# Kernel tuning notes

Hardware: AMD Instinct MI355X
Metric: run time of the kernel (lower is better)

Reference implementation:

```python
import jax, jax.numpy as jnp
import numpy as np

L, N, D_IN = 4, 2048, 1024
H, DH = 8, 64
INNER = H * DH          # 512
D_OUT = D_IN            # out_dim defaults to input_dim
SCALE = DH ** -0.5


def setup_inputs() -> dict:
    key = jax.random.key(0)
    ks = jax.random.split(key, 7)
    x = jax.random.normal(ks[0], (L, N, D_IN), jnp.float32)
    # torch Linear weights are [out_features, in_features]; xavier-ish scale
    Wq = jax.random.normal(ks[1], (INNER, D_IN), jnp.float32) * 0.03
    Wk = jax.random.normal(ks[2], (INNER, D_IN), jnp.float32) * 0.03
    Wv = jax.random.normal(ks[3], (INNER, D_IN), jnp.float32) * 0.03
    Wo = jax.random.normal(ks[4], (D_OUT, INNER), jnp.float32) * 0.03
    bo = jnp.zeros((D_OUT,), jnp.float32)
    # boolean key-padding mask [L, n]; ensure at least one valid key per row
    mask = jax.random.uniform(ks[5], (L, N)) < 0.9
    mask = mask.at[:, 0].set(True)
    return {"x": x, "Wq": Wq, "Wk": Wk, "Wv": Wv, "Wo": Wo, "bo": bo, "mask": mask}


def reference(x, Wq, Wk, Wv, Wo, bo, mask):
    # projections (Linear: y = x @ W^T), split heads: L n (h d) -> l h n d
    def split_heads(t):
        return t.reshape(L, N, H, DH).transpose(0, 2, 1, 3)

    q = split_heads(jnp.einsum('lnd,ed->lne', x, Wq))
    k = split_heads(jnp.einsum('lnd,ed->lne', x, Wk))  # context defaults to x
    v = split_heads(jnp.einsum('lnd,ed->lne', x, Wv))

    sim = jnp.einsum('lhnd,lhmd->lhnm', q, k) * SCALE   # [L,H,N,N]
    neg = -jnp.finfo(sim.dtype).max
    sim = jnp.where(mask[:, None, None, :], sim, neg)   # mask over key dim
    attn = jax.nn.softmax(sim, axis=-1)

    out = jnp.einsum('lhnm,lhmd->lhnd', attn, v)        # [L,H,N,DH]
    out = out.transpose(0, 2, 1, 3).reshape(L, N, INNER)
    return out @ Wo.T + bo                               # [L,N,D_OUT]
```

## Files before the change

### kernel.cpp

```cpp
#include <hip/hip_runtime.h>
#include <hip/hip_bf16.h>

#define L_DIM 4
#define N_DIM 2048
#define DIN   1024
#define H_DIM 8
#define DH    64
#define INNER 512

typedef __attribute__((ext_vector_type(8))) short short8;
typedef __attribute__((ext_vector_type(4))) float f32x4;

__device__ __forceinline__ unsigned short f2bf(float f) {
  unsigned u = __builtin_bit_cast(unsigned, f);
  u += 0x7fffu + ((u >> 16) & 1u);
  return (unsigned short)(u >> 16);
}

__device__ __forceinline__ unsigned pack2(float a, float b) {
  unsigned ua = __builtin_bit_cast(unsigned, a) + 0x8000u;
  unsigned ub = __builtin_bit_cast(unsigned, b) + 0x8000u;
  return (ua >> 16) | (ub & 0xffff0000u);
}

typedef __attribute__((address_space(3))) unsigned int lds_uint;
typedef const __attribute__((address_space(1))) unsigned int glob_uint;
__device__ __forceinline__ void gl_lds16(const unsigned short* g,
                                         unsigned short* l) {
  __builtin_amdgcn_global_load_lds((glob_uint*)g, (lds_uint*)l, 16, 0, 0);
}

__global__ void cast_all(const float* __restrict__ x,
                         const float* __restrict__ wq,
                         const float* __restrict__ wk,
                         const float* __restrict__ wv,
                         const float* __restrict__ wo,
                         unsigned short* __restrict__ xb,
                         unsigned short* __restrict__ w3,
                         unsigned short* __restrict__ wob,
                         const unsigned char* __restrict__ mraw,
                         float* __restrict__ bias) {
  __shared__ int votes[2];
  int bid = blockIdx.x, t = threadIdx.x;
  if (bid == 10240) {
    if (t < 2) votes[t] = 0;
    __syncthreads();
    const unsigned int* m32 = (const unsigned int*)mraw;
    int anyf = 0, any8 = 0;
    for (int i = t; i < 2048; i += 256) {
      unsigned w = m32[i];
      if (w == 0x3f800000u) anyf = 1;
      if (w & 0xffffff00u) any8 = 1;
    }
    if (anyf) atomicOr(&votes[0], 1);
    if (any8) atomicOr(&votes[1], 1);
    __syncthreads();
    int fmt = votes[0] ? 2 : (votes[1] ? 1 : 0);
    for (int i = t; i < L_DIM * N_DIM; i += 256) {
      int mv;
      if (fmt == 2)      mv = ((const float*)mraw)[i] != 0.0f;
      else if (fmt == 1) mv = mraw[i] != 0;
      else               mv = ((const int*)mraw)[i] != 0;
      bias[i] = mv ? 0.0f : -1e30f;
    }
    return;
  }
  int i = (bid * 256 + t) * 4;
  const float* src; unsigned short* dst; int off;
  if (i < 8388608)      { src = x;  dst = xb;           off = i; }
  else if (i < 8912896) { src = wq; dst = w3;           off = i - 8388608; }
  else if (i < 9437184) { src = wk; dst = w3 + 524288;  off = i - 8912896; }
  else if (i < 9961472) { src = wv; dst = w3 + 1048576; off = i - 9437184; }
  else                  { src = wo; dst = wob;          off = i - 9961472; }
  float4 f = *(const float4*)(src + off);
  ushort4 o4;
  o4.x = f2bf(f.x); o4.y = f2bf(f.y); o4.z = f2bf(f.z); o4.w = f2bf(f.w);
  *(ushort4*)(dst + off) = o4;
}

__launch_bounds__(256, 3)
__global__ void gemm_qkv(const unsigned short* __restrict__ xb,
                         const unsigned short* __restrict__ w3,
                         unsigned short* __restrict__ qp,
                         unsigned short* __restrict__ kp,
                         unsigned short* __restrict__ vtp) {
  __shared__ __align__(16) unsigned short Sh[8704];
  unsigned short* As = Sh;
  unsigned short* Bs = Sh + 4096;
  const int tid = threadIdx.x, lane = tid & 63, wid = tid >> 6;
  const int l16 = lane & 15, quad = lane >> 4;
  const int wm = wid >> 1, wn = wid & 1;
  const int m0 = blockIdx.x * 128, n0 = blockIdx.y * 128;

  f32x4 acc[4][4] = {};
  for (int kt = 0; kt < DIN; kt += 32) {
    __syncthreads();
#pragma unroll
    for (int it = 0; it < 2; ++it) {
      int c = it * 256 + wid * 64 + lane;
      int row = c >> 2, kseg = c & 3;
      unsigned short* lbase = &As[(it * 256 + wid * 64) * 8];
      gl_lds16(&xb[(m0 + row) * DIN + kt + kseg * 8], lbase);
      unsigned short* lbase2 = &Bs[(it * 256 + wid * 64) * 8];
      gl_lds16(&w3[(n0 + row) * DIN + kt + kseg * 8], lbase2);
    }
    __syncthreads();
    short8 af[4], bf[4];
#pragma unroll
    for (int mt = 0; mt < 4; ++mt)
      af[mt] = *(const short8*)&As[(wm * 64 + mt * 16 + l16) * 32 + quad * 8];
#pragma unroll
    for (int nt = 0; nt < 4; ++nt)
      bf[nt] = *(const short8*)&Bs[(wn * 64 + nt * 16 + l16) * 32 + quad * 8];
#pragma unroll
    for (int mt = 0; mt < 4; ++mt)
#pragma unroll
      for (int nt = 0; nt < 4; ++nt)
        acc[mt][nt] = __builtin_amdgcn_mfma_f32_16x16x32_bf16(
            af[mt], bf[nt], acc[mt][nt], 0, 0, 0);
  }
  if (blockIdx.y >= 8) {
    const int l = m0 >> 11, mloc = m0 & 2047;
#pragma unroll
    for (int chunk = 0; chunk < 2; ++chunk) {
      __syncthreads();
      if (wn == chunk) {
#pragma unroll
        for (int mt = 0; mt < 4; ++mt)
#pragma unroll
          for (int nt = 0; nt < 4; ++nt) {
            int col = nt * 16 + l16;
            int rowb = wm * 64 + mt * 16 + quad * 4;
            ushort4 pv;
            pv.x = f2bf(acc[mt][nt][0]);
            pv.y = f2bf(acc[mt][nt][1]);
            pv.z = f2bf(acc[mt][nt][2]);
            pv.w = f2bf(acc[mt][nt][3]);
            *(ushort4*)&Sh[col * 136 + rowb] = pv;
          }
      }
      __syncthreads();
      int hh = ((n0 + chunk * 64) & 511) >> 6;
#pragma unroll
      for (int it = 0; it < 4; ++it) {
        int c = it * 256 + tid;
        int cl = c >> 4, seg = c & 15;
        short8 vv = *(const short8*)&Sh[cl * 136 + seg * 8];
        *(short8*)&vtp[((size_t)((l * H_DIM + hh) * DH + cl)) * N_DIM + mloc +
                       seg * 8] = vv;
      }
    }
  } else {
#pragma unroll
    for (int mt = 0; mt < 4; ++mt)
#pragma unroll
      for (int nt = 0; nt < 4; ++nt)
#pragma unroll
        for (int r = 0; r < 4; ++r) {
          int grow = m0 + wm * 64 + mt * 16 + quad * 4 + r;
          int gcol = n0 + wn * 64 + nt * 16 + l16;
          unsigned short bv = f2bf(acc[mt][nt][r]);
          int h = (gcol & 511) >> 6, d = gcol & 63;
          int l = grow >> 11, n = grow & 2047;
          unsigned short* dst = (gcol >> 9) ? kp : qp;
          dst[(((l * H_DIM + h) * N_DIM + n) * DH) + d] = bv;
        }
  }
}

#define PW_S 64
__launch_bounds__(256, 2)
__global__ void attn_kernel(const unsigned short* __restrict__ qg,
                            const unsigned short* __restrict__ kg,
                            const unsigned short* __restrict__ vtg,
                            const float* __restrict__ bias,
                            unsigned short* __restrict__ aout) {
  __shared__ __align__(16) unsigned short Ks[2][128 * 64];
  __shared__ __align__(16) unsigned short Vs[2][64 * 128];
  __shared__ __align__(16) unsigned short Pw[128 * PW_S];
  const int tid = threadIdx.x, lane = tid & 63, wid = tid >> 6;
  const int l16 = lane & 15, quad = lane >> 4;
  const int bid = blockIdx.x;
  const int xcd = bid & 7, j = bid >> 3;
  const int lh = xcd * 4 + (j >> 4);
  const int q0 = (j & 15) << 7;
  const int l = lh >> 3, h = lh & 7;
  const unsigned short* Qb = qg + (size_t)lh * N_DIM * DH;
  const unsigned short* Kb = kg + (size_t)lh * N_DIM * DH;
  const unsigned short* Vt = vtg + (size_t)lh * DH * N_DIM;
  const float* bl = bias + l * N_DIM;

  short8 qf[2][2];
#pragma unroll
  for (int mt = 0; mt < 2; ++mt)
#pragma unroll
    for (int ks = 0; ks < 2; ++ks)
      qf[mt][ks] = *(const short8*)&Qb[(q0 + wid * 32 + mt * 16 + l16) * DH +
                                       ks * 32 + quad * 8];

  f32x4 o[2][4] = {};
  float lsum[2] = {0.f, 0.f};

#pragma unroll
  for (int it = 0; it < 4; ++it) {
    int cb = it * 256 + wid * 64;
    int c = cb + lane;
    int key = c >> 3, sl = c & 7, gs = (sl + key) & 7;
    gl_lds16(&Kb[key * DH + gs * 8], &Ks[0][cb * 8]);
    int d = c >> 4, sv = c & 15, gv = (sv + d) & 15;
    gl_lds16(&Vt[(size_t)d * N_DIM + gv * 8], &Vs[0][cb * 8]);
  }

  for (int t = 0; t < 16; ++t) {
    const int kv = t << 7, buf = t & 1;
    __syncthreads();
    if (t < 15) {
      int kv2 = kv + 128, b2 = buf ^ 1;
#pragma unroll
      for (int it = 0; it < 4; ++it) {
        int cb = it * 256 + wid * 64;
        int c = cb + lane;
        int key = c >> 3, sl = c & 7, gs = (sl + key) & 7;
        gl_lds16(&Kb[(kv2 + key) * DH + gs * 8], &Ks[b2][cb * 8]);
        int d = c >> 4, sv = c & 15, gv = (sv + d) & 15;
        gl_lds16(&Vt[(size_t)d * N_DIM + kv2 + gv * 8], &Vs[b2][cb * 8]);
      }
    }
    const unsigned short* Kst = Ks[buf];
    const unsigned short* Vst = Vs[buf];

#pragma unroll
    for (int hf = 0; hf < 2; ++hf) {
      f32x4 sc[2][4] = {};
#pragma unroll
      for (int nt = 0; nt < 4; ++nt)
#pragma unroll
        for (int ks = 0; ks < 2; ++ks) {
          int s = (ks * 4 + quad - l16) & 7;
          short8 kf = *(const short8*)&Kst[(hf * 64 + nt * 16 + l16) * 64 +
                                           s * 8];
#pragma unroll
          for (int mt = 0; mt < 2; ++mt)
            sc[mt][nt] = __builtin_amdgcn_mfma_f32_16x16x32_bf16(
                kf, qf[mt][ks], sc[mt][nt], 0, 0, 0);
        }
#pragma unroll
      for (int mt = 0; mt < 2; ++mt) {
        unsigned short* pr = &Pw[(wid * 32 + mt * 16 + l16) * PW_S];
#pragma unroll
        for (int nt = 0; nt < 4; ++nt) {
          float4 b4 = *(const float4*)&bl[kv + hf * 64 + nt * 16 + quad * 4];
          float p0 = __expf(fmaf(sc[mt][nt][0], 0.125f, b4.x));
          float p1 = __expf(fmaf(sc[mt][nt][1], 0.125f, b4.y));
          float p2 = __expf(fmaf(sc[mt][nt][2], 0.125f, b4.z));
          float p3 = __expf(fmaf(sc[mt][nt][3], 0.125f, b4.w));
          lsum[mt] += (p0 + p1) + (p2 + p3);
          uint2 pk = make_uint2(pack2(p0, p1), pack2(p2, p3));
          int gk = nt * 2 + (quad >> 1);
          int s = (gk + l16) & 7;
          *(uint2*)&pr[s * 8 + (quad & 1) * 4] = pk;
        }
      }
#pragma unroll
      for (int g = 0; g < 2; ++g) {
        short8 pa[2];
#pragma unroll
        for (int mt = 0; mt < 2; ++mt) {
          int sp = (g * 4 + quad + l16) & 7;
          pa[mt] = *(const short8*)&Pw[(wid * 32 + mt * 16 + l16) * PW_S +
                                       sp * 8];
        }
#pragma unroll
        for (int nt = 0; nt < 4; ++nt) {
          int dd = nt * 16 + l16;
          int sv2 = (hf * 8 + g * 4 + quad - l16) & 15;
          short8 vb = *(const short8*)&Vst[dd * 128 + sv2 * 8];
#pragma unroll
          for (int mt = 0; mt < 2; ++mt)
            o[mt][nt] = __builtin_amdgcn_mfma_f32_16x16x32_bf16(
                pa[mt], vb, o[mt][nt], 0, 0, 0);
        }
      }
    }
  }
#pragma unroll
  for (int mt = 0; mt < 2; ++mt) {
    lsum[mt] += __shfl_xor(lsum[mt], 16);
    lsum[mt] += __shfl_xor(lsum[mt], 32);
  }
#pragma unroll
  for (int mt = 0; mt < 2; ++mt)
#pragma unroll
    for (int r = 0; r < 4; ++r) {
      float inv = 1.f / __shfl(lsum[mt], quad * 4 + r);
      int row = q0 + wid * 32 + mt * 16 + quad * 4 + r;
#pragma unroll
      for (int nt = 0; nt < 4; ++nt)
        aout[(size_t)(l * N_DIM + row) * INNER + h * DH + nt * 16 + l16] =
            f2bf(o[mt][nt][r] * inv);
    }
}

__launch_bounds__(256, 3)
__global__ void gemm_out(const unsigned short* __restrict__ a,
                         const unsigned short* __restrict__ wo,
                         const float* __restrict__ bo,
                         float* __restrict__ out) {
  __shared__ unsigned short As[128 * 32];
  __shared__ unsigned short Bs[128 * 32];
  const int tid = threadIdx.x, lane = tid & 63, wid = tid >> 6;
  const int l16 = lane & 15, quad = lane >> 4;
  const int wm = wid >> 1, wn = wid & 1;
  const int m0 = blockIdx.x * 128, n0 = blockIdx.y * 128;

  f32x4 acc[4][4] = {};
  for (int kt = 0; kt < INNER; kt += 32) {
    __syncthreads();
#pragma unroll
    for (int it = 0; it < 2; ++it) {
      int c = it * 256 + wid * 64 + lane;
      int row = c >> 2, kseg = c & 3;
      unsigned short* lbase = &As[(it * 256 + wid * 64) * 8];
      gl_lds16(&a[(m0 + row) * INNER + kt + kseg * 8], lbase);
      unsigned short* lbase2 = &Bs[(it * 256 + wid * 64) * 8];
      gl_lds16(&wo[(n0 + row) * INNER + kt + kseg * 8], lbase2);
    }
    __syncthreads();
    short8 af[4], bf[4];
#pragma unroll
    for (int mt = 0; mt < 4; ++mt)
      af[mt] = *(const short8*)&As[(wm * 64 + mt * 16 + l16) * 32 + quad * 8];
#pragma unroll
    for (int nt = 0; nt < 4; ++nt)
      bf[nt] = *(const short8*)&Bs[(wn * 64 + nt * 16 + l16) * 32 + quad * 8];
#pragma unroll
    for (int mt = 0; mt < 4; ++mt)
#pragma unroll
      for (int nt = 0; nt < 4; ++nt)
        acc[mt][nt] = __builtin_amdgcn_mfma_f32_16x16x32_bf16(
            af[mt], bf[nt], acc[mt][nt], 0, 0, 0);
  }
#pragma unroll
  for (int mt = 0; mt < 4; ++mt)
#pragma unroll
    for (int nt = 0; nt < 4; ++nt)
#pragma unroll
      for (int r = 0; r < 4; ++r) {
        int grow = m0 + wm * 64 + mt * 16 + quad * 4 + r;
        int gcol = n0 + wn * 64 + nt * 16 + l16;
        out[(size_t)grow * DIN + gcol] = acc[mt][nt][r] + bo[gcol];
      }
}

extern "C" void kernel_launch(void* const* d_in, const int* in_sizes, int n_in,
                              void* d_out, int out_size, void* d_ws,
                              size_t ws_size, hipStream_t stream) {
  const float* x  = (const float*)d_in[0];
  const float* Wq = (const float*)d_in[1];
  const float* Wk = (const float*)d_in[2];
  const float* Wv = (const float*)d_in[3];
  const float* Wo = (const float*)d_in[4];
  const float* bo = (const float*)d_in[5];
  const unsigned char* mask = (const unsigned char*)d_in[6];
  float* out = (float*)d_out;

  char* ws = (char*)d_ws;
  unsigned short* xb  = (unsigned short*)(ws + 0);
  unsigned short* w3  = (unsigned short*)(ws + 16777216);
  unsigned short* wob = (unsigned short*)(ws + 19922944);
  unsigned short* q   = (unsigned short*)(ws + 20971520);
  unsigned short* k   = (unsigned short*)(ws + 29360128);
  unsigned short* vt  = (unsigned short*)(ws + 37748736);
  unsigned short* att = (unsigned short*)(ws + 46137344);
  float* bias         = (float*)(ws + 54525952);

  cast_all<<<10241, 256, 0, stream>>>(x, Wq, Wk, Wv, Wo, xb, w3, wob, mask,
                                      bias);
  gemm_qkv<<<dim3(64, 12), 256, 0, stream>>>(xb, w3, q, k, vt);
  attn_kernel<<<512, 256, 0, stream>>>(q, k, vt, bias, att);
  gemm_out<<<dim3(64, 8), 256, 0, stream>>>(att, wob, bo, out);
}
```

Before: 212.7 us.

## Double-buffer LDS tiles in projection GEMMs and use exp2 in softmax

Both the QKV projection GEMM and the output projection GEMM now use two LDS buffers. The next k-tile's global-to-LDS load is issued before the current tile's MFMAs, and each iteration needs only one barrier instead of two. The attention softmax replaces __expf with the hardware exp2 builtin, folding log2(e) into the scale constant. This doubles LDS per block in the GEMMs, which could limit occupancy. It relies on the barrier waiting for outstanding LDS-direct loads.

```diff
diff --git a/kernel.cpp b/kernel.cpp
--- a/kernel.cpp
+++ b/kernel.cpp
@@ -29,6 +29,8 @@
                                          unsigned short* l) {
   __builtin_amdgcn_global_load_lds((glob_uint*)g, (lds_uint*)l, 16, 0, 0);
 }
+
+#define SCL2 0.18033688011112042f
 
 __global__ void cast_all(const float* __restrict__ x,
                          const float* __restrict__ wq,
@@ -84,27 +86,40 @@
                          unsigned short* __restrict__ qp,
                          unsigned short* __restrict__ kp,
                          unsigned short* __restrict__ vtp) {
-  __shared__ __align__(16) unsigned short Sh[8704];
-  unsigned short* As = Sh;
-  unsigned short* Bs = Sh + 4096;
+  __shared__ __align__(16) unsigned short Sh[16384];
   const int tid = threadIdx.x, lane = tid & 63, wid = tid >> 6;
   const int l16 = lane & 15, quad = lane >> 4;
   const int wm = wid >> 1, wn = wid & 1;
   const int m0 = blockIdx.x * 128, n0 = blockIdx.y * 128;
 
+#pragma unroll
+  for (int it = 0; it < 2; ++it) {
+    int c = it * 256 + wid * 64 + lane;
+    int row = c >> 2, kseg = c & 3;
+    gl_lds16(&xb[(m0 + row) * DIN + kseg * 8],
+             &Sh[(it * 256 + wid * 64) * 8]);
+    gl_lds16(&w3[(n0 + row) * DIN + kseg * 8],
+             &Sh[4096 + (it * 256 + wid * 64) * 8]);
+  }
+
   f32x4 acc[4][4] = {};
-  for (int kt = 0; kt < DIN; kt += 32) {
+  for (int t = 0; t < 32; ++t) {
+    const int boff = (t & 1) ? 8192 : 0;
     __syncthreads();
-#pragma unroll
-    for (int it = 0; it < 2; ++it) {
-      int c = it * 256 + wid * 64 + lane;
-      int row = c >> 2, kseg = c & 3;
-      unsigned short* lbase = &As[(it * 256 + wid * 64) * 8];
-      gl_lds16(&xb[(m0 + row) * DIN + kt + kseg * 8], lbase);
-      unsigned short* lbase2 = &Bs[(it * 256 + wid * 64) * 8];
-      gl_lds16(&w3[(n0 + row) * DIN + kt + kseg * 8], lbase2);
-    }
-    __syncthreads();
+    if (t < 31) {
+      const int kt2 = (t + 1) * 32, b2 = boff ^ 8192;
+#pragma unroll
+      for (int it = 0; it < 2; ++it) {
+        int c = it * 256 + wid * 64 + lane;
+        int row = c >> 2, kseg = c & 3;
+        gl_lds16(&xb[(m0 + row) * DIN + kt2 + kseg * 8],
+                 &Sh[b2 + (it * 256 + wid * 64) * 8]);
+        gl_lds16(&w3[(n0 + row) * DIN + kt2 + kseg * 8],
+                 &Sh[b2 + 4096 + (it * 256 + wid * 64) * 8]);
+      }
+    }
+    const unsigned short* As = &Sh[boff];
+    const unsigned short* Bs = &Sh[boff + 4096];
     short8 af[4], bf[4];
 #pragma unroll
     for (int mt = 0; mt < 4; ++mt)
@@ -250,10 +265,10 @@
 #pragma unroll
         for (int nt = 0; nt < 4; ++nt) {
           float4 b4 = *(const float4*)&bl[kv + hf * 64 + nt * 16 + quad * 4];
-          float p0 = __expf(fmaf(sc[mt][nt][0], 0.125f, b4.x));
-          float p1 = __expf(fmaf(sc[mt][nt][1], 0.125f, b4.y));
-          float p2 = __expf(fmaf(sc[mt][nt][2], 0.125f, b4.z));
-          float p3 = __expf(fmaf(sc[mt][nt][3], 0.125f, b4.w));
+          float p0 = __builtin_amdgcn_exp2f(fmaf(sc[mt][nt][0], SCL2, b4.x));
+          float p1 = __builtin_amdgcn_exp2f(fmaf(sc[mt][nt][1], SCL2, b4.y));
+          float p2 = __builtin_amdgcn_exp2f(fmaf(sc[mt][nt][2], SCL2, b4.z));
+          float p3 = __builtin_amdgcn_exp2f(fmaf(sc[mt][nt][3], SCL2, b4.w));
           lsum[mt] += (p0 + p1) + (p2 + p3);
           uint2 pk = make_uint2(pack2(p0, p1), pack2(p2, p3));
           int gk = nt * 2 + (quad >> 1);
@@ -306,26 +321,40 @@
                          const unsigned short* __restrict__ wo,
                          const float* __restrict__ bo,
                          float* __restrict__ out) {
-  __shared__ unsigned short As[128 * 32];
-  __shared__ unsigned short Bs[128 * 32];
+  __shared__ __align__(16) unsigned short Sh[16384];
   const int tid = threadIdx.x, lane = tid & 63, wid = tid >> 6;
   const int l16 = lane & 15, quad = lane >> 4;
   const int wm = wid >> 1, wn = wid & 1;
   const int m0 = blockIdx.x * 128, n0 = blockIdx.y * 128;
 
+#pragma unroll
+  for (int it = 0; it < 2; ++it) {
+    int c = it * 256 + wid * 64 + lane;
+    int row = c >> 2, kseg = c & 3;
+    gl_lds16(&a[(m0 + row) * INNER + kseg * 8],
+             &Sh[(it * 256 + wid * 64) * 8]);
+    gl_lds16(&wo[(n0 + row) * INNER + kseg * 8],
+             &Sh[4096 + (it * 256 + wid * 64) * 8]);
+  }
+
   f32x4 acc[4][4] = {};
-  for (int kt = 0; kt < INNER; kt += 32) {
+  for (int t = 0; t < 16; ++t) {
+    const int boff = (t & 1) ? 8192 : 0;
     __syncthreads();
-#pragma unroll
-    for (int it = 0; it < 2; ++it) {
-      int c = it * 256 + wid * 64 + lane;
-      int row = c >> 2, kseg = c & 3;
-      unsigned short* lbase = &As[(it * 256 + wid * 64) * 8];
-      gl_lds16(&a[(m0 + row) * INNER + kt + kseg * 8], lbase);
-      unsigned short* lbase2 = &Bs[(it * 256 + wid * 64) * 8];
-      gl_lds16(&wo[(n0 + row) * INNER + kt + kseg * 8], lbase2);
-    }
-    __syncthreads();
+    if (t < 15) {
+      const int kt2 = (t + 1) * 32, b2 = boff ^ 8192;
+#pragma unroll
+      for (int it = 0; it < 2; ++it) {
+        int c = it * 256 + wid * 64 + lane;
+        int row = c >> 2, kseg = c & 3;
+        gl_lds16(&a[(m0 + row) * INNER + kt2 + kseg * 8],
+                 &Sh[b2 + (it * 256 + wid * 64) * 8]);
+        gl_lds16(&wo[(n0 + row) * INNER + kt2 + kseg * 8],
+                 &Sh[b2 + 4096 + (it * 256 + wid * 64) * 8]);
+      }
+    }
+    const unsigned short* As = &Sh[boff];
+    const unsigned short* Bs = &Sh[boff + 4096];
     short8 af[4], bf[4];
 #pragma unroll
     for (int mt = 0; mt < 4; ++mt)
```

Measured after the change: 219.2 us. +3.0%, slower.
